# Optimization experiments

Measured on AMD Instinct MI355X. Metric: run time of the kernel, lower is better.

## Reference

```python
import jax, jax.numpy as jnp
import numpy as np

NUM_CLASSES = 41
TEMP = 0.1
EPS = 1e-12  # torch F.normalize eps


def setup_inputs() -> dict:
    key = jax.random.key(0)
    k1, k2, k3 = jax.random.split(key, 3)
    B, C, H, W = 8, 128, 160, 160
    features_s = jax.random.normal(k1, (B, C, H, W), dtype=jnp.float32)
    features_t = jax.random.normal(k2, (B, C, H, W), dtype=jnp.float32)
    labels = jax.random.randint(k3, (B, H, W), 0, NUM_CLASSES, dtype=jnp.int32)
    return {"features_s": features_s, "features_t": features_t, "labels": labels}


def _class_vectors(feat, lab_flat, row, R, C):
    # Replicates: (feat * mask_cl).view(-1, C).sum(-1) / C for every class.
    # Each flat element f of feat belongs to class lab_flat[f] and row r = f // C.
    # v[cl, r] = sum of flat elements in chunk r with label cl, divided by C.
    flat = feat.reshape(-1)  # [B*C*H*W]
    v = jnp.zeros((NUM_CLASSES, R), dtype=feat.dtype)
    v = v.at[lab_flat, row].add(flat)
    return v / C


def _l2norm_rows(x):
    # torch F.normalize(p=2, dim=0) on each 1D class vector -> per-row L2 norm here
    n = jnp.sqrt(jnp.sum(x * x, axis=1, keepdims=True))
    return x / jnp.maximum(n, EPS)


def reference(features_s, features_t, labels):
    B, C, H, W = features_s.shape
    R = B * H * W  # == B*C*H*W // C, length of each per-class vector
    F_ = B * C * H * W

    # label of every flat feature element (labels broadcast over channel axis)
    lab_full = jnp.broadcast_to(labels[:, None, :, :], (B, C, H, W)).reshape(-1)
    row = jnp.arange(F_, dtype=jnp.int32) // C  # flat-chunk index per element

    v_s = _class_vectors(features_s, lab_full, row, R, C)  # [K, R]
    v_t = _class_vectors(features_t, lab_full, row, R, C)  # [K, R]

    Sn = _l2norm_rows(v_s)
    Tn = _l2norm_rows(v_t)

    logits = jnp.matmul(Sn, Tn.T) / TEMP  # [K, K]

    # classes present in labels (absent classes have zero rows and are skipped)
    counts = jnp.zeros((NUM_CLASSES,), dtype=jnp.int32).at[labels.reshape(-1)].add(1)
    present = counts > 0

    diag = jnp.diagonal(logits)
    lse = jax.nn.logsumexp(logits, axis=1)  # log(sum_j exp(logits[i, j]))
    terms = -(diag - lse)  # -log(exp(diag) / rowsum)
    loss = jnp.sum(jnp.where(present, terms, 0.0)) / jnp.sum(present).astype(logits.dtype)
    return loss
```

## Files before the change

### kernel.cpp

```cpp
#include <hip/hip_runtime.h>

#define KCL 41
#define BB 8
#define CC 128
#define HWSZ 25600
#define PP 200
#define TSTR 33
#define ASTR 132

__global__ __launch_bounds__(256) void init_ws(float* ws) {
    for (int i = threadIdx.x; i < KCL * KCL + 3 * KCL; i += 256) ws[i] = 0.f;
}

__global__ __launch_bounds__(256) void main_k(const float* __restrict__ fs,
                                              const float* __restrict__ ft,
                                              const int* __restrict__ labels,
                                              float* __restrict__ G,
                                              float* __restrict__ NS,
                                              float* __restrict__ NT,
                                              int* __restrict__ CNT)
{
    __shared__ int lab[128];
    __shared__ unsigned long long mask64[2][KCL];
    __shared__ __align__(16) float tile[2][CC][TSTR];
    __shared__ __align__(16) float A[2][KCL][ASTR];

    const int bp = blockIdx.x;
    const int b = bp / PP, p = bp % PP;
    const int tid = threadIdx.x;

    {
        float* a0 = &A[0][0][0];
        for (int i = tid; i < 2 * KCL * ASTR; i += 256) a0[i] = 0.f;
    }
    if (tid < 128) lab[tid] = labels[b * HWSZ + p * 128 + tid];
    __syncthreads();

    const int wv = tid >> 6, ln = tid & 63;
    if (wv < 2) {
        int myl = lab[(wv << 6) + ln];
        for (int cl = 0; cl < KCL; ++cl) {
            unsigned long long mm = __ballot(myl == cl);
            if (ln == 0) mask64[wv][cl] = mm;
        }
    }
    __syncthreads();
    if (tid < KCL)
        atomicAdd(&CNT[tid], (int)(__popcll(mask64[0][tid]) + __popcll(mask64[1][tid])));

    const int tn = tid >> 7;
    const int c  = tid & 127;
    const size_t base_s = (size_t)b * CC * HWSZ + (size_t)p * 128;

    float4 ld[8];
    #pragma unroll
    for (int k = 0; k < 8; ++k) {
        int ch = tid + (k << 8);
        int tns = ch >> 10, cs = (ch >> 3) & 127, j4 = ch & 7;
        const float* f = tns ? ft : fs;
        ld[k] = *(const float4*)(f + base_s + (size_t)cs * HWSZ + (j4 << 2));
    }

    for (int s = 0; s < 4; ++s) {
        __syncthreads();
        #pragma unroll
        for (int k = 0; k < 8; ++k) {
            int ch = tid + (k << 8);
            int tns = ch >> 10, cs = (ch >> 3) & 127, j4 = ch & 7;
            float* dst = &tile[tns][cs][j4 << 2];
            dst[0] = ld[k].x; dst[1] = ld[k].y; dst[2] = ld[k].z; dst[3] = ld[k].w;
        }
        if (s < 3) {
            #pragma unroll
            for (int k = 0; k < 8; ++k) {
                int ch = tid + (k << 8);
                int tns = ch >> 10, cs = (ch >> 3) & 127, j4 = ch & 7;
                const float* f = tns ? ft : fs;
                ld[k] = *(const float4*)(f + base_s + (size_t)cs * HWSZ + ((s + 1) * 32 + (j4 << 2)));
            }
        }
        __syncthreads();
        {
            const float* trow = &tile[tn][c][0];
            const int half = s >> 1, sh = (s & 1) << 5;
            for (int cl = 0; cl < KCL; ++cl) {
                unsigned mm = (unsigned)(mask64[half][cl] >> sh);
                if (!mm) continue;
                float sum = 0.f;
                do { int j = __builtin_ctz(mm); mm &= mm - 1; sum += trow[j]; } while (mm);
                A[tn][cl][c] += sum;
            }
        }
    }
    __syncthreads();

    {
        const int ti = tid >> 4, tj = tid & 15;
        float acc[3][3] = {};
        for (int c4 = 0; c4 < 32; ++c4) {
            float4 av[3], bv[3];
            #pragma unroll
            for (int u = 0; u < 3; ++u) {
                int I = ti + (u << 4); if (I > KCL - 1) I = KCL - 1;
                int J = tj + (u << 4); if (J > KCL - 1) J = KCL - 1;
                av[u] = *(const float4*)(&A[0][I][c4 << 2]);
                bv[u] = *(const float4*)(&A[1][J][c4 << 2]);
            }
            #pragma unroll
            for (int u = 0; u < 3; ++u)
                #pragma unroll
                for (int v = 0; v < 3; ++v)
                    acc[u][v] += av[u].x * bv[v].x + av[u].y * bv[v].y
                               + av[u].z * bv[v].z + av[u].w * bv[v].w;
        }
        #pragma unroll
        for (int u = 0; u < 3; ++u) {
            int I = ti + (u << 4); if (I >= KCL) continue;
            #pragma unroll
            for (int v = 0; v < 3; ++v) {
                int J = tj + (v << 4); if (J >= KCL) continue;
                atomicAdd(&G[I * KCL + J], acc[u][v]);
            }
        }
    }

    if (tid < KCL) {
        float ss = 0.f, tt = 0.f;
        for (int c4 = 0; c4 < 32; ++c4) {
            float4 a  = *(const float4*)(&A[0][tid][c4 << 2]);
            float4 b2 = *(const float4*)(&A[1][tid][c4 << 2]);
            ss += a.x * a.x + a.y * a.y + a.z * a.z + a.w * a.w;
            tt += b2.x * b2.x + b2.y * b2.y + b2.z * b2.z + b2.w * b2.w;
        }
        atomicAdd(&NS[tid], ss);
        atomicAdd(&NT[tid], tt);
    }
}

__global__ void finalize(const float* __restrict__ G,
                         const float* __restrict__ NS,
                         const float* __restrict__ NT,
                         const int* __restrict__ CNT,
                         float* __restrict__ out)
{
    __shared__ float sn[KCL], tnn[KCL];
    const int t = threadIdx.x;
    if (t < KCL) {
        sn[t]  = fmaxf(sqrtf(NS[t]), 1e-12f);
        tnn[t] = fmaxf(sqrtf(NT[t]), 1e-12f);
    }
    __syncthreads();
    float term = 0.f; int pres = 0;
    if (t < KCL) {
        const float inv = 10.f / sn[t];
        float l[KCL];
        float mx = -1e30f, diag = 0.f;
        #pragma unroll
        for (int j = 0; j < KCL; ++j) {
            l[j] = G[t * KCL + j] * inv / tnn[j];
            if (l[j] > mx) mx = l[j];
            if (j == t) diag = l[j];
        }
        float s = 0.f;
        #pragma unroll
        for (int j = 0; j < KCL; ++j) s += expf(l[j] - mx);
        float lse = logf(s) + mx;
        pres = (CNT[t] > 0) ? 1 : 0;
        term = pres ? (lse - diag) : 0.f;
    }
    #pragma unroll
    for (int off = 32; off > 0; off >>= 1) {
        term += __shfl_down(term, off);
        pres += __shfl_down(pres, off);
    }
    if (t == 0) out[0] = term / (float)pres;
}

extern "C" void kernel_launch(void* const* d_in, const int* in_sizes, int n_in,
                              void* d_out, int out_size, void* d_ws, size_t ws_size,
                              hipStream_t stream) {
    const float* fs     = (const float*)d_in[0];
    const float* ft     = (const float*)d_in[1];
    const int*   labels = (const int*)d_in[2];
    float* G  = (float*)d_ws;
    float* NS = G + KCL * KCL;
    float* NT = NS + KCL;
    int*   CNT = (int*)(NT + KCL);
    float* out = (float*)d_out;

    hipLaunchKernelGGL(init_ws, dim3(1), dim3(256), 0, stream, G);
    hipLaunchKernelGGL(main_k, dim3(BB * PP), dim3(256), 0, stream,
                       fs, ft, labels, G, NS, NT, CNT);
    hipLaunchKernelGGL(finalize, dim3(1), dim3(64), 0, stream, G, NS, NT, CNT, out);
}
```

Baseline: 322.3 us.

## Replace shared tile and bitmask scan with direct LDS atomic scatter into class accumulators

Drops the staged shared-memory tile and the per-class ballot-mask scan. Each thread now loads float4 pixels per channel and atomically adds each value into the class/channel accumulator in LDS, using labels packed four to a word. This removes the double-buffered staging, the per-stage barriers and the 41-class loop per channel. In exchange it issues many LDS float atomics, which can contend when nearby pixels share a class, and it no longer overlaps the global loads with compute.

```diff
diff --git a/kernel.cpp b/kernel.cpp
--- a/kernel.cpp
+++ b/kernel.cpp
@@ -5,7 +5,6 @@
 #define CC 128
 #define HWSZ 25600
 #define PP 200
-#define TSTR 33
 #define ASTR 132
 
 __global__ __launch_bounds__(256) void init_ws(float* ws) {
@@ -21,8 +20,8 @@
                                               int* __restrict__ CNT)
 {
     __shared__ int lab[128];
+    __shared__ unsigned lab4b[32];
     __shared__ unsigned long long mask64[2][KCL];
-    __shared__ __align__(16) float tile[2][CC][TSTR];
     __shared__ __align__(16) float A[2][KCL][ASTR];
 
     const int bp = blockIdx.x;
@@ -36,6 +35,10 @@
     if (tid < 128) lab[tid] = labels[b * HWSZ + p * 128 + tid];
     __syncthreads();
 
+    if (tid < 32)
+        lab4b[tid] = (unsigned)lab[4 * tid] | ((unsigned)lab[4 * tid + 1] << 8)
+                   | ((unsigned)lab[4 * tid + 2] << 16) | ((unsigned)lab[4 * tid + 3] << 24);
+
     const int wv = tid >> 6, ln = tid & 63;
     if (wv < 2) {
         int myl = lab[(wv << 6) + ln];
@@ -48,49 +51,29 @@
     if (tid < KCL)
         atomicAdd(&CNT[tid], (int)(__popcll(mask64[0][tid]) + __popcll(mask64[1][tid])));
 
-    const int tn = tid >> 7;
-    const int c  = tid & 127;
-    const size_t base_s = (size_t)b * CC * HWSZ + (size_t)p * 128;
+    const unsigned labs = lab4b[tid & 31];
+    const int cl0 = labs & 255, cl1 = (labs >> 8) & 255,
+              cl2 = (labs >> 16) & 255, cl3 = (labs >> 24) & 255;
+    const int c0 = tid >> 5;
+    const size_t base_g = (size_t)b * CC * HWSZ + (size_t)p * 128 + (size_t)((tid & 31) << 2);
 
-    float4 ld[8];
     #pragma unroll
-    for (int k = 0; k < 8; ++k) {
-        int ch = tid + (k << 8);
-        int tns = ch >> 10, cs = (ch >> 3) & 127, j4 = ch & 7;
-        const float* f = tns ? ft : fs;
-        ld[k] = *(const float4*)(f + base_s + (size_t)cs * HWSZ + (j4 << 2));
+    for (int k = 0; k < 16; ++k) {
+        const int c = (k << 3) + c0;
+        float4 v = *(const float4*)(fs + base_g + (size_t)c * HWSZ);
+        atomicAdd(&A[0][cl0][c], v.x);
+        atomicAdd(&A[0][cl1][c], v.y);
+        atomicAdd(&A[0][cl2][c], v.z);
+        atomicAdd(&A[0][cl3][c], v.w);
     }
-
-    for (int s = 0; s < 4; ++s) {
-        __syncthreads();
-        #pragma unroll
-        for (int k = 0; k < 8; ++k) {
-            int ch = tid + (k << 8);
-            int tns = ch >> 10, cs = (ch >> 3) & 127, j4 = ch & 7;
-            float* dst = &tile[tns][cs][j4 << 2];
-            dst[0] = ld[k].x; dst[1] = ld[k].y; dst[2] = ld[k].z; dst[3] = ld[k].w;
-        }
-        if (s < 3) {
-            #pragma unroll
-            for (int k = 0; k < 8; ++k) {
-                int ch = tid + (k << 8);
-                int tns = ch >> 10, cs = (ch >> 3) & 127, j4 = ch & 7;
-                const float* f = tns ? ft : fs;
-                ld[k] = *(const float4*)(f + base_s + (size_t)cs * HWSZ + ((s + 1) * 32 + (j4 << 2)));
-            }
-        }
-        __syncthreads();
-        {
-            const float* trow = &tile[tn][c][0];
-            const int half = s >> 1, sh = (s & 1) << 5;
-            for (int cl = 0; cl < KCL; ++cl) {
-                unsigned mm = (unsigned)(mask64[half][cl] >> sh);
-                if (!mm) continue;
-                float sum = 0.f;
-                do { int j = __builtin_ctz(mm); mm &= mm - 1; sum += trow[j]; } while (mm);
-                A[tn][cl][c] += sum;
-            }
-        }
+    #pragma unroll
+    for (int k = 0; k < 16; ++k) {
+        const int c = (k << 3) + c0;
+        float4 v = *(const float4*)(ft + base_g + (size_t)c * HWSZ);
+        atomicAdd(&A[1][cl0][c], v.x);
+        atomicAdd(&A[1][cl1][c], v.y);
+        atomicAdd(&A[1][cl2][c], v.z);
+        atomicAdd(&A[1][cl3][c], v.w);
     }
     __syncthreads();
 
```

Measured after the change: 488.5 us. +51.6%, slower.
